# Kernel optimization log

Hardware: AMD Instinct MI355X
Metric: run time of the kernel (lower is better)

The kernel has to match this reference:

```python
import jax, jax.numpy as jnp
import numpy as np

B, S, D_MODEL, H = 4, 2048, 1024, 16
DEPTH = D_MODEL // H          # 64
HD = DEPTH // 2               # 32, per-head projection dim
SCALE = float(np.sqrt(DEPTH))  # note: sqrt(full depth), as in the torch code
NEG = -1e10


def setup_inputs() -> dict:
    key = jax.random.key(0)
    kq, kk, kv, km, kwq, kwk, kwv, kwo = jax.random.split(key, 8)
    q = jax.random.normal(kq, (B, S, D_MODEL), dtype=jnp.float32)
    k = jax.random.normal(kk, (B, S, D_MODEL), dtype=jnp.float32)
    v = jax.random.normal(kv, (B, S, D_MODEL), dtype=jnp.float32)
    attention_mask = jax.random.uniform(km, (B, S, S)) < 0.1
    # xavier-uniform-ish init; stacked per-head weights [H, d_model, hd]
    lim_qkv = float(np.sqrt(6.0 / (D_MODEL + HD)))
    Wq = jax.random.uniform(kwq, (H, D_MODEL, HD), minval=-lim_qkv, maxval=lim_qkv)
    Wk = jax.random.uniform(kwk, (H, D_MODEL, HD), minval=-lim_qkv, maxval=lim_qkv)
    Wv = jax.random.uniform(kwv, (H, D_MODEL, HD), minval=-lim_qkv, maxval=lim_qkv)
    lim_o = float(np.sqrt(6.0 / (H * HD + D_MODEL)))
    Wo = jax.random.uniform(kwo, (H * HD, D_MODEL), minval=-lim_o, maxval=lim_o)
    return {"q": q, "k": k, "v": v, "attention_mask": attention_mask,
            "Wq": Wq, "Wk": Wk, "Wv": Wv, "Wo": Wo}


def reference(q, k, v, attention_mask, Wq, Wk, Wv, Wo):
    # batched per-head projections (equivalent to the per-head Linear loop)
    Q = jnp.einsum('bsd,hde->bhse', q, Wq)   # [B,H,S,hd]
    K = jnp.einsum('bsd,hde->bhse', k, Wk)
    V = jnp.einsum('bsd,hde->bhse', v, Wv)
    scores = jnp.einsum('bhqe,bhke->bhqk', Q, K) / SCALE  # [B,H,S,S]
    scores = jnp.where(attention_mask[:, None, :, :], NEG, scores)
    attn = jax.nn.softmax(scores, axis=-1)
    z = jnp.einsum('bhqk,bhke->bhqe', attn, V)            # [B,H,S,hd]
    # concat heads along last dim (head order matches torch cat)
    multi = z.transpose(0, 2, 1, 3).reshape(q.shape[0], q.shape[1], H * HD)
    out = multi @ Wo                                       # [B,S,d_model]
    return out  # dropout p=0.0 (eval) is identity
```

## Files before the change

kernel.cpp:

```cpp
#include <hip/hip_runtime.h>
#include <hip/hip_bf16.h>
#include <math.h>

typedef unsigned short u16;
typedef unsigned int u32;
typedef __attribute__((ext_vector_type(8))) short s16x8;
typedef __attribute__((ext_vector_type(4))) short s16x4;
typedef __attribute__((ext_vector_type(4))) float f32x4;
typedef __attribute__((ext_vector_type(16))) float f32x16;

#define DEV static __device__ __forceinline__

DEV u16 f2bf(float f){
  __hip_bfloat16 h = __float2bfloat16(f);
  return *reinterpret_cast<u16*>(&h);
}

DEV u32 cvt_pk_bf16(float lo, float hi_){
  u32 r;
  asm("v_cvt_pk_bf16_f32 %0, %1, %2" : "=v"(r) : "v"(lo), "v"(hi_));
  return r;
}

__global__ void detect_mask_kernel(const unsigned char* __restrict__ m, int* __restrict__ flag){
  __shared__ int cnt;
  if (threadIdx.x==0) cnt=0;
  __syncthreads();
  int nz=0;
  for (int i=threadIdx.x;i<4096;i+=256) nz += (m[(size_t)i*4+1]!=0)?1:0;
  if (nz) atomicAdd(&cnt, nz);
  __syncthreads();
  if (threadIdx.x==0) *flag = (cnt==0)?4:1;
}

__global__ __launch_bounds__(256) void pack_mask_kernel(const unsigned char* __restrict__ m,
    const int* __restrict__ flag, u16* __restrict__ mb16){
  const int stride = *flag;
  const size_t gid = (size_t)blockIdx.x*256u + threadIdx.x;
  u32 bits = 0;
  if (stride == 1){
    const uint4 v = *(const uint4*)(m + gid*16);
    bits  =  ((v.x & 0x01010101u) * 0x01020408u) >> 24;
    bits |= (((v.y & 0x01010101u) * 0x01020408u) >> 24) << 4;
    bits |= (((v.z & 0x01010101u) * 0x01020408u) >> 24) << 8;
    bits |= (((v.w & 0x01010101u) * 0x01020408u) >> 24) << 12;
  } else {
    const unsigned char* mm = m + gid*64;
    const uint4 a = *(const uint4*)(mm);
    const uint4 b = *(const uint4*)(mm+16);
    const uint4 c = *(const uint4*)(mm+32);
    const uint4 d = *(const uint4*)(mm+48);
    bits  = (u32)(a.x!=0) | ((u32)(a.y!=0)<<1) | ((u32)(a.z!=0)<<2) | ((u32)(a.w!=0)<<3)
          | ((u32)(b.x!=0)<<4) | ((u32)(b.y!=0)<<5) | ((u32)(b.z!=0)<<6) | ((u32)(b.w!=0)<<7)
          | ((u32)(c.x!=0)<<8) | ((u32)(c.y!=0)<<9) | ((u32)(c.z!=0)<<10)| ((u32)(c.w!=0)<<11)
          | ((u32)(d.x!=0)<<12)| ((u32)(d.y!=0)<<13)| ((u32)(d.z!=0)<<14)| ((u32)(d.w!=0)<<15);
  }
  mb16[gid] = (u16)bits;
}

__global__ __launch_bounds__(256) void prep_weights_kernel(
    const float* __restrict__ Wq, const float* __restrict__ Wk, const float* __restrict__ Wv,
    const float* __restrict__ Wo, u16* __restrict__ WT, u16* __restrict__ WoT){
  int gid = blockIdx.x*256 + threadIdx.x;
  if (gid < 3*512*1024){
    int z = gid >> 19;
    int r = gid & ((1<<19)-1);
    int n = r >> 10, d = r & 1023;
    const float* W = (z==0)?Wq:((z==1)?Wk:Wv);
    int h = n>>5, e = n&31;
    float wv = W[((size_t)h*1024 + (size_t)d)*32 + e];
    if (z==0) wv *= 0.18033688011112042f;
    WT[gid] = f2bf(wv);
  } else {
    int r = gid - 3*512*1024;
    int n = r >> 9, cc = r & 511;
    WoT[r] = f2bf(Wo[(size_t)cc*1024 + n]);
  }
}

__global__ __launch_bounds__(256) void gemm_proj_kernel(
    const float* __restrict__ Aq, const float* __restrict__ Ak, const float* __restrict__ Av,
    const u16* __restrict__ WT, u16* __restrict__ Qp, u16* __restrict__ Kp, u16* __restrict__ Vt)
{
  __shared__ u16 As[128*64];
  __shared__ u16 Bs[128*64];
  const int z = blockIdx.z;
  const float* __restrict__ A = (z==0)?Aq:((z==1)?Ak:Av);
  const u16* __restrict__ W = WT + (size_t)z*(512*1024);
  const int m0 = blockIdx.x*128, n0 = blockIdx.y*128;
  const int t = threadIdx.x, lane = t&63, wv = t>>6;
  const int wr = wv>>1, wc = wv&1;
  const int c = lane&15, g = lane>>4;
  f32x4 acc[4][4] = {};
  for (int kk=0; kk<1024; kk+=64){
    #pragma unroll
    for (int j=0;j<8;j++){
      int idx = t + j*256;
      int row = idx>>4, kq=(idx&15)<<2;
      f32x4 a4 = *(const f32x4*)(A + (size_t)(m0+row)*1024 + kk + kq);
      s16x4 b4;
      b4[0]=(short)f2bf(a4[0]); b4[1]=(short)f2bf(a4[1]);
      b4[2]=(short)f2bf(a4[2]); b4[3]=(short)f2bf(a4[3]);
      int co = (kq<<1) ^ ((row&7)<<4);
      *(s16x4*)((char*)As + row*128 + co) = b4;
    }
    #pragma unroll
    for (int j=0;j<4;j++){
      int idx = t + j*256;
      int n = idx>>3, k8=(idx&7)<<3;
      s16x8 bv = *(const s16x8*)(W + (size_t)(n0+n)*1024 + kk + k8);
      int co = (k8<<1) ^ ((n&7)<<4);
      *(s16x8*)((char*)Bs + n*128 + co) = bv;
    }
    __syncthreads();
    #pragma unroll
    for (int ks=0;ks<2;ks++){
      s16x8 af[4], bf[4];
      #pragma unroll
      for (int i=0;i<4;i++){
        int ra = wr*64 + i*16 + c;
        af[i] = *(const s16x8*)((const char*)As + ra*128 + ((ks*64 + g*16) ^ ((ra&7)<<4)));
        int rb = wc*64 + i*16 + c;
        bf[i] = *(const s16x8*)((const char*)Bs + rb*128 + ((ks*64 + g*16) ^ ((rb&7)<<4)));
      }
      #pragma unroll
      for (int mi=0;mi<4;mi++)
        #pragma unroll
        for (int nj=0;nj<4;nj++)
          acc[mi][nj] = __builtin_amdgcn_mfma_f32_16x16x32_bf16(af[mi], bf[nj], acc[mi][nj], 0, 0, 0);
    }
    __syncthreads();
  }
  #pragma unroll
  for (int mi=0;mi<4;mi++){
    #pragma unroll
    for (int nj=0;nj<4;nj++){
      #pragma unroll
      for (int r=0;r<4;r++){
        int gm = m0 + wr*64 + mi*16 + g*4 + r;
        int gn = n0 + wc*64 + nj*16 + c;
        u16 val = f2bf(acc[mi][nj][r]);
        int b = gm>>11, s = gm&2047, hh = gn>>5, e = gn&31;
        if (z==0)      Qp[((size_t)(b*16+hh)*2048 + s)*32 + e] = val;
        else if (z==1) Kp[((size_t)(b*16+hh)*2048 + s)*32 + e] = val;
        else           Vt[((size_t)(b*16+hh)*32 + e)*2048 + s] = val;
      }
    }
  }
}

__global__ __launch_bounds__(256, 4) void attn_kernel(
    const u16* __restrict__ Qp, const u16* __restrict__ Kp, const u16* __restrict__ Vt,
    const u32* __restrict__ mb32, u16* __restrict__ Z)
{
  __shared__ float Osh[4][32][36];
  const int t = threadIdx.x, lane = t&63, wid = t>>6;
  const int c = lane&31, hi = lane>>5;
  const int hi8 = hi*8;
  const int wg = blockIdx.x;
  const int xcd = wg & 7, loc = wg >> 3;
  const int bh = xcd*8 + (loc>>4);
  const int qb = loc & 15;
  const int b = bh>>4, h = bh&15;
  const int q0 = qb*128 + wid*32;
  const u16* Qh = Qp + (size_t)bh*2048*32;
  const u16* Kh = Kp + (size_t)bh*2048*32;
  const u16* Vh = Vt + (size_t)bh*32*2048;

  const s16x8 qf0 = *(const s16x8*)(Qh + (size_t)(q0 + c)*32 + hi8);
  const s16x8 qf1 = *(const s16x8*)(Qh + (size_t)(q0 + c)*32 + 16 + hi8);

  const f32x16 z16 = {0,0,0,0,0,0,0,0,0,0,0,0,0,0,0,0};
  f32x16 O = z16;
  float mrun = -INFINITY, lrun = 0.f;
  const u32* mrowp = mb32 + ((size_t)b*2048 + (size_t)(q0 + c))*64;

  for (int kb=0; kb<2048; kb+=32){
    const s16x8 kf0 = *(const s16x8*)(Kh + (size_t)(kb + c)*32 + hi8);
    const s16x8 kf1 = *(const s16x8*)(Kh + (size_t)(kb + c)*32 + 16 + hi8);
    const s16x8 vf0 = *(const s16x8*)(Vh + (size_t)c*2048 + kb + hi8);
    const s16x8 vf1 = *(const s16x8*)(Vh + (size_t)c*2048 + kb + 16 + hi8);
    const u32 mw = mrowp[kb>>5];

    f32x16 p = __builtin_amdgcn_mfma_f32_32x32x16_bf16(kf0, qf0, z16, 0, 0, 0);
    p = __builtin_amdgcn_mfma_f32_32x32x16_bf16(kf1, qf1, p, 0, 0, 0);

    const u32 ms = mw >> (4*hi);
    #pragma unroll
    for (int r=0;r<16;r++){
      const int cpos = (r&3) + 8*(r>>2);
      if ((ms >> cpos) & 1u) p[r] = -1e10f;
    }
    float mx8[8];
    #pragma unroll
    for (int i=0;i<8;i++) mx8[i] = fmaxf(p[i], p[i+8]);
    #pragma unroll
    for (int i=0;i<4;i++) mx8[i] = fmaxf(mx8[i], mx8[i+4]);
    float mx = fmaxf(fmaxf(mx8[0],mx8[1]), fmaxf(mx8[2],mx8[3]));
    mx = fmaxf(mx, __shfl_xor(mx, 32));
    const float nm = fmaxf(mrun, mx);
    const float fr = exp2f(mrun - nm);
    mrun = nm;
    #pragma unroll
    for (int r=0;r<16;r++) p[r] = exp2f(p[r] - nm);
    float s8[8];
    #pragma unroll
    for (int i=0;i<8;i++) s8[i] = p[i] + p[i+8];
    #pragma unroll
    for (int i=0;i<4;i++) s8[i] += s8[i+4];
    float own = (s8[0]+s8[1]) + (s8[2]+s8[3]);
    const float rs = own + __shfl_xor(own, 32);
    lrun = lrun*fr + rs;
    #pragma unroll
    for (int r=0;r<16;r++) O[r] *= fr;

    u32 pw[8], sw[8];
    #pragma unroll
    for (int u=0;u<8;u++) pw[u] = cvt_pk_bf16(p[2*u], p[2*u+1]);
    #pragma unroll
    for (int u=0;u<8;u++) sw[u] = __shfl_xor(pw[u], 32);
    const bool hb = (hi != 0);
    union { u32 u[4]; s16x8 v; } bf0, bf1;
    bf0.u[0] = hb ? sw[2] : pw[0];
    bf0.u[1] = hb ? sw[3] : pw[1];
    bf0.u[2] = hb ? pw[2] : sw[0];
    bf0.u[3] = hb ? pw[3] : sw[1];
    bf1.u[0] = hb ? sw[6] : pw[4];
    bf1.u[1] = hb ? sw[7] : pw[5];
    bf1.u[2] = hb ? pw[6] : sw[4];
    bf1.u[3] = hb ? pw[7] : sw[5];

    O = __builtin_amdgcn_mfma_f32_32x32x16_bf16(vf0, bf0.v, O, 0, 0, 0);
    O = __builtin_amdgcn_mfma_f32_32x32x16_bf16(vf1, bf1.v, O, 0, 0, 0);
  }

  const float linv = 1.0f / lrun;
  #pragma unroll
  for (int r=0;r<16;r++){
    const int hd = (r&3) + 8*(r>>2) + 4*hi;
    Osh[wid][c][hd] = O[r] * linv;
  }
  __syncthreads();
  const int rq = lane >> 1, rc0 = (lane & 1)*16;
  const float* orow = &Osh[wid][rq][0];
  union { u16 q[8]; s16x8 v; } o0, o1;
  #pragma unroll
  for (int j=0;j<8;j++){ o0.q[j] = f2bf(orow[rc0+j]); o1.q[j] = f2bf(orow[rc0+8+j]); }
  u16* zp = Z + ((size_t)b*2048 + (size_t)(q0 + rq))*512 + h*32 + rc0;
  *(s16x8*)(zp)   = o0.v;
  *(s16x8*)(zp+8) = o1.v;
}

__global__ __launch_bounds__(256) void gemm_out_kernel(
    const u16* __restrict__ Zb, const u16* __restrict__ WoT, float* __restrict__ out)
{
  __shared__ u16 As[128*64];
  __shared__ u16 Bs[128*64];
  const int m0 = blockIdx.x*128, n0 = blockIdx.y*128;
  const int t = threadIdx.x, lane=t&63, wv=t>>6;
  const int wr=wv>>1, wc=wv&1, c=lane&15, g=lane>>4;
  f32x4 acc[4][4] = {};
  for (int kk=0; kk<512; kk+=64){
    #pragma unroll
    for (int j=0;j<4;j++){
      int idx = t + j*256;
      int row = idx>>3, k8=(idx&7)<<3;
      int co = (k8<<1) ^ ((row&7)<<4);
      s16x8 av = *(const s16x8*)(Zb + (size_t)(m0+row)*512 + kk + k8);
      *(s16x8*)((char*)As + row*128 + co) = av;
      s16x8 bv = *(const s16x8*)(WoT + (size_t)(n0+row)*512 + kk + k8);
      *(s16x8*)((char*)Bs + row*128 + co) = bv;
    }
    __syncthreads();
    #pragma unroll
    for (int ks=0;ks<2;ks++){
      s16x8 af[4], bf[4];
      #pragma unroll
      for (int i=0;i<4;i++){
        int ra = wr*64 + i*16 + c;
        af[i] = *(const s16x8*)((const char*)As + ra*128 + ((ks*64 + g*16) ^ ((ra&7)<<4)));
        int rb = wc*64 + i*16 + c;
        bf[i] = *(const s16x8*)((const char*)Bs + rb*128 + ((ks*64 + g*16) ^ ((rb&7)<<4)));
      }
      #pragma unroll
      for (int mi=0;mi<4;mi++)
        #pragma unroll
        for (int nj=0;nj<4;nj++)
          acc[mi][nj] = __builtin_amdgcn_mfma_f32_16x16x32_bf16(af[mi], bf[nj], acc[mi][nj], 0, 0, 0);
    }
    __syncthreads();
  }
  #pragma unroll
  for (int mi=0;mi<4;mi++)
    #pragma unroll
    for (int nj=0;nj<4;nj++)
      #pragma unroll
      for (int r=0;r<4;r++){
        int gm = m0 + wr*64 + mi*16 + g*4 + r;
        int gn = n0 + wc*64 + nj*16 + c;
        out[(size_t)gm*1024 + gn] = acc[mi][nj][r];
      }
}

extern "C" void kernel_launch(void* const* d_in, const int* in_sizes, int n_in,
                              void* d_out, int out_size, void* d_ws, size_t ws_size,
                              hipStream_t stream)
{
  const float* q  = (const float*)d_in[0];
  const float* k  = (const float*)d_in[1];
  const float* v  = (const float*)d_in[2];
  const unsigned char* mask = (const unsigned char*)d_in[3];
  const float* Wq = (const float*)d_in[4];
  const float* Wk = (const float*)d_in[5];
  const float* Wv = (const float*)d_in[6];
  const float* Wo = (const float*)d_in[7];
  float* out = (float*)d_out;

  char* ws = (char*)d_ws;
  u16* Qp  = (u16*)(ws);
  u16* Kp  = (u16*)(ws + 8388608);
  u16* Vt  = (u16*)(ws + 16777216);
  u16* Z   = (u16*)(ws + 25165824);
  u16* WT  = (u16*)(ws + 33554432);
  u16* WoT = (u16*)(ws + 36700160);
  u16* mb16 = (u16*)(ws + 37748736);
  int* flag = (int*)(ws + 39845888);

  detect_mask_kernel<<<1, 256, 0, stream>>>(mask, flag);
  pack_mask_kernel<<<4096, 256, 0, stream>>>(mask, flag, mb16);
  prep_weights_kernel<<<8192, 256, 0, stream>>>(Wq, Wk, Wv, Wo, WT, WoT);
  gemm_proj_kernel<<<dim3(64,4,3), 256, 0, stream>>>(q, k, v, WT, Qp, Kp, Vt);
  attn_kernel<<<1024, 256, 0, stream>>>(Qp, Kp, Vt, (const u32*)mb16, Z);
  gemm_out_kernel<<<dim3(64,8), 256, 0, stream>>>(Z, WoT, out);
  (void)in_sizes; (void)n_in; (void)out_size; (void)ws_size;
}
```

Measured before the change: 236.0 us.

## Widen attention tiles to 64 keys, prefetch K, use permlane32 swaps and lazy rescale

The flash-attention inner loop now handles 64 keys per step as two 32-key MFMA tiles and double-buffers the K fragments and mask words one tile ahead. The cross-half max/sum reductions and the P-fragment reshuffle use v_permlane32_swap instead of __shfl_xor plus selects. The running-max rescale of O and l is skipped unless some lane's max rises by more than 8, and exp2f is replaced by the hardware exp2 builtin. The aim is to cut shuffle, rescale and load-latency overhead per key, at the cost of more registers and a thresholded online softmax.

```diff
diff --git a/kernel.cpp b/kernel.cpp
--- a/kernel.cpp
+++ b/kernel.cpp
@@ -4,10 +4,12 @@
 
 typedef unsigned short u16;
 typedef unsigned int u32;
+typedef unsigned long long u64;
 typedef __attribute__((ext_vector_type(8))) short s16x8;
 typedef __attribute__((ext_vector_type(4))) short s16x4;
 typedef __attribute__((ext_vector_type(4))) float f32x4;
 typedef __attribute__((ext_vector_type(16))) float f32x16;
+typedef __attribute__((ext_vector_type(2))) unsigned int u32x2;
 
 #define DEV static __device__ __forceinline__
 
@@ -20,6 +22,18 @@
   u32 r;
   asm("v_cvt_pk_bf16_f32 %0, %1, %2" : "=v"(r) : "v"(lo), "v"(hi_));
   return r;
+}
+
+DEV u32x2 pl32swap(u32 a, u32 b){
+  return __builtin_amdgcn_permlane32_swap(a, b, false, false);
+}
+DEV float xhalf_max(float x){
+  u32x2 r = pl32swap(__float_as_uint(x), __float_as_uint(x));
+  return fmaxf(__uint_as_float(r[0]), __uint_as_float(r[1]));
+}
+DEV float xhalf_sum(float x){
+  u32x2 r = pl32swap(__float_as_uint(x), __float_as_uint(x));
+  return __uint_as_float(r[0]) + __uint_as_float(r[1]);
 }
 
 __global__ void detect_mask_kernel(const unsigned char* __restrict__ m, int* __restrict__ flag){
@@ -175,63 +189,97 @@
   float mrun = -INFINITY, lrun = 0.f;
   const u32* mrowp = mb32 + ((size_t)b*2048 + (size_t)(q0 + c))*64;
 
-  for (int kb=0; kb<2048; kb+=32){
-    const s16x8 kf0 = *(const s16x8*)(Kh + (size_t)(kb + c)*32 + hi8);
-    const s16x8 kf1 = *(const s16x8*)(Kh + (size_t)(kb + c)*32 + 16 + hi8);
-    const s16x8 vf0 = *(const s16x8*)(Vh + (size_t)c*2048 + kb + hi8);
-    const s16x8 vf1 = *(const s16x8*)(Vh + (size_t)c*2048 + kb + 16 + hi8);
-    const u32 mw = mrowp[kb>>5];
-
-    f32x16 p = __builtin_amdgcn_mfma_f32_32x32x16_bf16(kf0, qf0, z16, 0, 0, 0);
-    p = __builtin_amdgcn_mfma_f32_32x32x16_bf16(kf1, qf1, p, 0, 0, 0);
-
-    const u32 ms = mw >> (4*hi);
+  auto loadK4 = [&](int kb, s16x8 &f0, s16x8 &f1, s16x8 &f2, s16x8 &f3){
+    const u16* kbase = Kh + (size_t)(kb + c)*32 + hi8;
+    f0 = *(const s16x8*)(kbase);
+    f1 = *(const s16x8*)(kbase + 16);
+    f2 = *(const s16x8*)(kbase + 1024);
+    f3 = *(const s16x8*)(kbase + 1040);
+  };
+
+  auto tile = [&](const s16x8 &kf0, const s16x8 &kf1, const s16x8 &kf2, const s16x8 &kf3,
+                  int kb, u32 mA, u32 mB){
+    const u16* vbase = Vh + (size_t)c*2048 + kb + hi8;
+    const s16x8 vf0 = *(const s16x8*)(vbase);
+    const s16x8 vf1 = *(const s16x8*)(vbase + 16);
+    const s16x8 vf2 = *(const s16x8*)(vbase + 32);
+    const s16x8 vf3 = *(const s16x8*)(vbase + 48);
+
+    f32x16 p0 = __builtin_amdgcn_mfma_f32_32x32x16_bf16(kf0, qf0, z16, 0, 0, 0);
+    p0 = __builtin_amdgcn_mfma_f32_32x32x16_bf16(kf1, qf1, p0, 0, 0, 0);
+    f32x16 p1 = __builtin_amdgcn_mfma_f32_32x32x16_bf16(kf2, qf0, z16, 0, 0, 0);
+    p1 = __builtin_amdgcn_mfma_f32_32x32x16_bf16(kf3, qf1, p1, 0, 0, 0);
+
+    const u32 msA = mA >> (4*hi), msB = mB >> (4*hi);
     #pragma unroll
     for (int r=0;r<16;r++){
       const int cpos = (r&3) + 8*(r>>2);
-      if ((ms >> cpos) & 1u) p[r] = -1e10f;
-    }
-    float mx8[8];
-    #pragma unroll
-    for (int i=0;i<8;i++) mx8[i] = fmaxf(p[i], p[i+8]);
-    #pragma unroll
-    for (int i=0;i<4;i++) mx8[i] = fmaxf(mx8[i], mx8[i+4]);
-    float mx = fmaxf(fmaxf(mx8[0],mx8[1]), fmaxf(mx8[2],mx8[3]));
-    mx = fmaxf(mx, __shfl_xor(mx, 32));
-    const float nm = fmaxf(mrun, mx);
-    const float fr = exp2f(mrun - nm);
-    mrun = nm;
-    #pragma unroll
-    for (int r=0;r<16;r++) p[r] = exp2f(p[r] - nm);
+      if ((msA >> cpos) & 1u) p0[r] = -1e10f;
+      if ((msB >> cpos) & 1u) p1[r] = -1e10f;
+    }
+    float m8[8];
+    #pragma unroll
+    for (int i=0;i<8;i++) m8[i] = fmaxf(fmaxf(p0[i], p0[i+8]), fmaxf(p1[i], p1[i+8]));
+    #pragma unroll
+    for (int i=0;i<4;i++) m8[i] = fmaxf(m8[i], m8[i+4]);
+    float mx = fmaxf(fmaxf(m8[0],m8[1]), fmaxf(m8[2],m8[3]));
+    mx = xhalf_max(mx);
+
+    if (__any(mx > mrun + 8.f)){
+      const float nm = fmaxf(mrun, mx);
+      const float fr = __builtin_amdgcn_exp2f(mrun - nm);
+      mrun = nm;
+      lrun *= fr;
+      #pragma unroll
+      for (int r=0;r<16;r++) O[r] *= fr;
+    }
+    #pragma unroll
+    for (int r=0;r<16;r++){
+      p0[r] = __builtin_amdgcn_exp2f(p0[r] - mrun);
+      p1[r] = __builtin_amdgcn_exp2f(p1[r] - mrun);
+    }
     float s8[8];
     #pragma unroll
-    for (int i=0;i<8;i++) s8[i] = p[i] + p[i+8];
+    for (int i=0;i<8;i++) s8[i] = (p0[i] + p0[i+8]) + (p1[i] + p1[i+8]);
     #pragma unroll
     for (int i=0;i<4;i++) s8[i] += s8[i+4];
     float own = (s8[0]+s8[1]) + (s8[2]+s8[3]);
-    const float rs = own + __shfl_xor(own, 32);
-    lrun = lrun*fr + rs;
-    #pragma unroll
-    for (int r=0;r<16;r++) O[r] *= fr;
-
-    u32 pw[8], sw[8];
-    #pragma unroll
-    for (int u=0;u<8;u++) pw[u] = cvt_pk_bf16(p[2*u], p[2*u+1]);
-    #pragma unroll
-    for (int u=0;u<8;u++) sw[u] = __shfl_xor(pw[u], 32);
-    const bool hb = (hi != 0);
-    union { u32 u[4]; s16x8 v; } bf0, bf1;
-    bf0.u[0] = hb ? sw[2] : pw[0];
-    bf0.u[1] = hb ? sw[3] : pw[1];
-    bf0.u[2] = hb ? pw[2] : sw[0];
-    bf0.u[3] = hb ? pw[3] : sw[1];
-    bf1.u[0] = hb ? sw[6] : pw[4];
-    bf1.u[1] = hb ? sw[7] : pw[5];
-    bf1.u[2] = hb ? pw[6] : sw[4];
-    bf1.u[3] = hb ? pw[7] : sw[5];
-
-    O = __builtin_amdgcn_mfma_f32_32x32x16_bf16(vf0, bf0.v, O, 0, 0, 0);
-    O = __builtin_amdgcn_mfma_f32_32x32x16_bf16(vf1, bf1.v, O, 0, 0, 0);
+    lrun += xhalf_sum(own);
+
+    u32 pwA[8], pwB[8];
+    #pragma unroll
+    for (int u=0;u<8;u++){ pwA[u] = cvt_pk_bf16(p0[2*u], p0[2*u+1]); pwB[u] = cvt_pk_bf16(p1[2*u], p1[2*u+1]); }
+    u32x2 a02 = pl32swap(pwA[0], pwA[2]);
+    u32x2 a13 = pl32swap(pwA[1], pwA[3]);
+    u32x2 a46 = pl32swap(pwA[4], pwA[6]);
+    u32x2 a57 = pl32swap(pwA[5], pwA[7]);
+    u32x2 b02 = pl32swap(pwB[0], pwB[2]);
+    u32x2 b13 = pl32swap(pwB[1], pwB[3]);
+    u32x2 b46 = pl32swap(pwB[4], pwB[6]);
+    u32x2 b57 = pl32swap(pwB[5], pwB[7]);
+    union { u32 u[4]; s16x8 v; } fA0 = {{a02[0], a13[0], a02[1], a13[1]}};
+    union { u32 u[4]; s16x8 v; } fA1 = {{a46[0], a57[0], a46[1], a57[1]}};
+    union { u32 u[4]; s16x8 v; } fB0 = {{b02[0], b13[0], b02[1], b13[1]}};
+    union { u32 u[4]; s16x8 v; } fB1 = {{b46[0], b57[0], b46[1], b57[1]}};
+
+    O = __builtin_amdgcn_mfma_f32_32x32x16_bf16(vf0, fA0.v, O, 0, 0, 0);
+    O = __builtin_amdgcn_mfma_f32_32x32x16_bf16(vf1, fA1.v, O, 0, 0, 0);
+    O = __builtin_amdgcn_mfma_f32_32x32x16_bf16(vf2, fB0.v, O, 0, 0, 0);
+    O = __builtin_amdgcn_mfma_f32_32x32x16_bf16(vf3, fB1.v, O, 0, 0, 0);
+  };
+
+  s16x8 ka0, ka1, ka2, ka3;
+  loadK4(0, ka0, ka1, ka2, ka3);
+  u64 mwa = *(const u64*)(mrowp);
+  for (int kb = 0; kb < 2048; kb += 128){
+    s16x8 kb0, kb1, kb2, kb3;
+    loadK4(kb + 64, kb0, kb1, kb2, kb3);
+    u64 mwb = *(const u64*)(mrowp + ((kb + 64) >> 5));
+    tile(ka0, ka1, ka2, ka3, kb, (u32)mwa, (u32)(mwa >> 32));
+    const int nxt = (kb + 128) & 2047;
+    loadK4(nxt, ka0, ka1, ka2, ka3);
+    mwa = *(const u64*)(mrowp + (nxt >> 5));
+    tile(kb0, kb1, kb2, kb3, kb + 64, (u32)mwb, (u32)(mwb >> 32));
   }
 
   const float linv = 1.0f / lrun;
```

Measured after the change: 208.9 us. 1.13x faster.
